# Performance work log

Hardware: AMD Instinct MI355X
Metric: run time of the kernel (lower is better)

Reference implementation:

```python
import jax, jax.numpy as jnp
import numpy as np

N_QUBITS = 10
DIM = 2 ** N_QUBITS
W_MUL = (2.0 ** 0.5) * 5.0 ** (-0.5)  # he_std * lrmul, use_wscale=True, lrmul=1
MEASURE_QUBIT = 5


def _c(v):
    return v.astype(jnp.complex64)


def _m2(a, b, c, d):
    return jnp.stack([jnp.stack([a, b]), jnp.stack([c, d])])


_ZERO = jnp.zeros((), jnp.complex64)


def _rx(phi):
    c, s = _c(jnp.cos(phi / 2)), _c(jnp.sin(phi / 2))
    return _m2(c, -1j * s, -1j * s, c)


def _ry(phi):
    c, s = _c(jnp.cos(phi / 2)), _c(jnp.sin(phi / 2))
    return _m2(c, -s, s, c)


def _rz(phi):
    c, s = _c(jnp.cos(phi / 2)), _c(jnp.sin(phi / 2))
    return _m2(c - 1j * s, _ZERO, _ZERO, c + 1j * s)


_CNOT = jnp.array([[1, 0, 0, 0], [0, 1, 0, 0], [0, 0, 0, 1], [0, 0, 1, 0]], jnp.complex64)


def _expand(g, n, q):
    # kron(I_{2^q}, g, I_{2^{n-q-k}}) where g acts on qubits q..q+k-1
    k = int(np.log2(g.shape[0]))
    left = jnp.eye(2 ** q, dtype=jnp.complex64)
    right = jnp.eye(2 ** (n - q - k), dtype=jnp.complex64)
    return jnp.kron(left, jnp.kron(g, right))


def _layer_unitary(weight):
    w = weight * W_MUL
    U = jnp.eye(DIM, dtype=jnp.complex64)
    for sign in (1.0, -1.0):
        for q in range(N_QUBITS):
            U = _expand(_rx(sign * w[q]), N_QUBITS, q) @ U
            U = _expand(_ry(sign * w[q + 10]), N_QUBITS, q) @ U
            U = _expand(_rz(sign * w[q + 20]), N_QUBITS, q) @ U
        for q in range(1, N_QUBITS):
            U = _expand(_CNOT, N_QUBITS, q - 1) @ U
    return U


def _measure_affinity(rho, which_q):
    # Tr(rho @ Z_which_q) with Z_q = kron(I, Z, I); Z_q is diagonal
    z = jnp.array([1.0, -1.0], jnp.float32)
    zdiag = jnp.kron(jnp.ones(2 ** which_q, jnp.float32),
                     jnp.kron(z, jnp.ones(2 ** (N_QUBITS - which_q - 1), jnp.float32)))
    return jnp.sum(jnp.diagonal(rho).real * zdiag).astype(jnp.float32)


def setup_inputs() -> dict:
    key = jax.random.key(0)
    k1, k2 = jax.random.split(key)
    x = jax.random.normal(k1, (DIM, DIM), dtype=jnp.float32)
    weight = jax.random.uniform(k2, (30,), dtype=jnp.float32, minval=0.0, maxval=2.0 * np.pi)
    return {"x": x, "weight": weight}


def reference(x, weight):
    E = _layer_unitary(weight)
    rho = (E @ x.astype(jnp.complex64)) @ E.conj().T
    return _measure_affinity(rho, MEASURE_QUBIT)
```

## Files before the change

kernel.cpp:

```cpp
#include <hip/hip_runtime.h>

#define DIM 1024
#define NQ 10

__device__ __forceinline__ float2 cmul(float2 a, float2 b) {
    return make_float2(a.x * b.x - a.y * b.y, a.x * b.y + a.y * b.x);
}
__device__ __forceinline__ float2 cadd(float2 a, float2 b) {
    return make_float2(a.x + b.x, a.y + b.y);
}
__device__ __forceinline__ float2 csub(float2 a, float2 b) {
    return make_float2(a.x - b.x, a.y - b.y);
}
__device__ __forceinline__ float2 cconj(float2 a) { return make_float2(a.x, -a.y); }

__device__ __forceinline__ void mm2(const float2* A, const float2* B, float2* C) {
    C[0] = cadd(cmul(A[0], B[0]), cmul(A[1], B[2]));
    C[1] = cadd(cmul(A[0], B[1]), cmul(A[1], B[3]));
    C[2] = cadd(cmul(A[2], B[0]), cmul(A[3], B[2]));
    C[3] = cadd(cmul(A[2], B[1]), cmul(A[3], B[3]));
}

__device__ __forceinline__ void compute_gates(const float* __restrict__ weight,
                                              float2* G, float2* Msh, int tid) {
    if (tid < NQ) {
        int q = tid;
        const float WM = 0.632455532033676f;
        float px = weight[q]      * WM * 0.5f;
        float py = weight[q + 10] * WM * 0.5f;
        float pz = weight[q + 20] * WM * 0.5f;
        float cx = cosf(px), sx = sinf(px);
        float cy = cosf(py), sy = sinf(py);
        float cz = cosf(pz), sz = sinf(pz);
        {
            float2 Rx[4] = { {cx, 0.f}, {0.f, -sx}, {0.f, -sx}, {cx, 0.f} };
            float2 Ry[4] = { {cy, 0.f}, {-sy, 0.f}, {sy, 0.f}, {cy, 0.f} };
            float2 Rz[4] = { {cz, -sz}, {0.f, 0.f}, {0.f, 0.f}, {cz, sz} };
            float2 T[4], u[4];
            mm2(Ry, Rx, T);
            mm2(Rz, T, u);
            G[q * 4 + 0] = u[0]; G[q * 4 + 1] = u[1];
            G[q * 4 + 2] = u[2]; G[q * 4 + 3] = u[3];
        }
        if (Msh && q < 6) {
            float nsx = -sx, nsy = -sy, nsz = -sz;
            float2 Rx[4] = { {cx, 0.f}, {0.f, -nsx}, {0.f, -nsx}, {cx, 0.f} };
            float2 Ry[4] = { {cy, 0.f}, {-nsy, 0.f}, {nsy, 0.f}, {cy, 0.f} };
            float2 Rz[4] = { {cz, -nsz}, {0.f, 0.f}, {0.f, 0.f}, {cz, nsz} };
            float2 T[4], u2[4];
            mm2(Ry, Rx, T);
            mm2(Rz, T, u2);
            for (int i = 0; i < 2; i++)
                for (int j = 0; j < 2; j++) {
                    float2 v = csub(cmul(cconj(u2[0 * 2 + i]), u2[0 * 2 + j]),
                                    cmul(cconj(u2[1 * 2 + i]), u2[1 * 2 + j]));
                    Msh[q * 4 + i * 2 + j] = v;
                }
        }
    }
}

__global__ __launch_bounds__(256) void pass1(const float* __restrict__ x,
                                             const float* __restrict__ weight,
                                             float2* __restrict__ z,
                                             float* __restrict__ out) {
    __shared__ float2 G[40];
    int tid = threadIdx.x;
    compute_gates(weight, G, nullptr, tid);
    __syncthreads();
    if (blockIdx.x == 0 && tid == 0) out[0] = 0.f;

    int lane = tid & 63;
    int r = blockIdx.x * 4 + (tid >> 6);
    const float4* xp = (const float4*)(x + r * DIM + lane * 16);
    float2 v[16];
#pragma unroll
    for (int k = 0; k < 4; k++) {
        float4 a = xp[k];
        v[k * 4 + 0] = make_float2(a.x, 0.f);
        v[k * 4 + 1] = make_float2(a.y, 0.f);
        v[k * 4 + 2] = make_float2(a.z, 0.f);
        v[k * 4 + 3] = make_float2(a.w, 0.f);
    }
#pragma unroll
    for (int q = 0; q < 6; q++) {
        float2 u0 = cconj(G[q * 4]),     u1 = cconj(G[q * 4 + 1]);
        float2 u2 = cconj(G[q * 4 + 2]), u3 = cconj(G[q * 4 + 3]);
        const int X = 1 << (5 - q);
        bool up = (lane & X) != 0;
        float2 go = up ? u3 : u0;
        float2 gp = up ? u2 : u1;
#pragma unroll
        for (int j = 0; j < 16; j++) {
            float2 p;
            p.x = __shfl_xor(v[j].x, X, 64);
            p.y = __shfl_xor(v[j].y, X, 64);
            v[j] = cadd(cmul(go, v[j]), cmul(gp, p));
        }
    }
#pragma unroll
    for (int q = 6; q < 10; q++) {
        float2 u0 = cconj(G[q * 4]),     u1 = cconj(G[q * 4 + 1]);
        float2 u2 = cconj(G[q * 4 + 2]), u3 = cconj(G[q * 4 + 3]);
        const int h = 1 << (9 - q);
#pragma unroll
        for (int j0 = 0; j0 < 16; j0++) {
            if ((j0 & h) == 0) {
                int j1 = j0 | h;
                float2 s0 = v[j0], s1 = v[j1];
                v[j0] = cadd(cmul(u0, s0), cmul(u1, s1));
                v[j1] = cadd(cmul(u2, s0), cmul(u3, s1));
            }
        }
    }
    float4* zp = (float4*)(z + r * DIM + lane * 16);
#pragma unroll
    for (int k = 0; k < 8; k++)
        zp[k] = make_float4(v[2 * k].x, v[2 * k].y, v[2 * k + 1].x, v[2 * k + 1].y);
}

__device__ __forceinline__ float extract_half(int c, const float2 v[8], int half,
                                              int lane, const float2* Msh) {
    int af = c;
    af ^= af >> 1; af ^= af >> 2; af ^= af >> 4; af ^= af >> 8;
    int t = af & 15;
    int a05 = af >> 4;
    float2 m6 = make_float2(1.f, 0.f);
#pragma unroll
    for (int q = 0; q < 6; q++) {
        int ia = (a05 >> (5 - q)) & 1;
        int ib = (lane >> (5 - q)) & 1;
        m6 = cmul(m6, Msh[q * 4 + ia * 2 + ib]);
    }
    int pl = lane;
    pl ^= pl >> 1; pl ^= pl >> 2; pl ^= pl >> 4;
    float acc = 0.f;
#pragma unroll
    for (int jj = 0; jj < 8; jj++) {
        int j = half * 8 + jj;
        int p4j = j ^ (j >> 1) ^ (j >> 2) ^ (j >> 3);
        int parmask = (p4j & 1) ? 63 : 0;
        int bf = (p4j << 6) | (pl ^ parmask);
        int b05 = bf >> 4;
        float mx = __shfl(m6.x, b05, 64);
        float my = __shfl(m6.y, b05, 64);
        if ((bf & 15) == t) acc += mx * v[jj].x - my * v[jj].y;
    }
    return acc;
}

__global__ __launch_bounds__(256) void pass2(const float2* __restrict__ z,
                                             const float* __restrict__ weight,
                                             float* __restrict__ out) {
    __shared__ float2 G[40];
    __shared__ float2 Msh[24];
    __shared__ float2 ex[2 * 2 * 8 * 2 * 64];
    __shared__ float part[4];
    int tid = threadIdx.x;
    int lane = tid & 63;
    int w = tid >> 6;
    int pair = w >> 1;
    int half = w & 1;
    int c0 = blockIdx.x * 4 + pair * 2;

    float2 v0[8], v1[8];
#pragma unroll
    for (int jj = 0; jj < 8; jj++) {
        int j = half * 8 + jj;
        float4 t = *(const float4*)(z + ((j << 6) + lane) * DIM + c0);
        v0[jj] = make_float2(t.x, t.y);
        v1[jj] = make_float2(t.z, t.w);
    }
    compute_gates(weight, G, Msh, tid);
    int sec = pair * 2 + half;
#pragma unroll
    for (int jj = 0; jj < 8; jj++) {
        ex[((sec * 8 + jj) * 2 + 0) * 64 + lane] = v0[jj];
        ex[((sec * 8 + jj) * 2 + 1) * 64 + lane] = v1[jj];
    }
    __syncthreads();
    {
        float2 u0 = G[0], u1 = G[1], u2 = G[2], u3 = G[3];
        float2 go = half ? u3 : u0;
        float2 gp = half ? u2 : u1;
        int other = pair * 2 + (1 - half);
#pragma unroll
        for (int jj = 0; jj < 8; jj++) {
            float2 p0 = ex[((other * 8 + jj) * 2 + 0) * 64 + lane];
            float2 p1 = ex[((other * 8 + jj) * 2 + 1) * 64 + lane];
            v0[jj] = cadd(cmul(go, v0[jj]), cmul(gp, p0));
            v1[jj] = cadd(cmul(go, v1[jj]), cmul(gp, p1));
        }
    }
#pragma unroll
    for (int q = 1; q < 4; q++) {
        float2 u0 = G[q * 4], u1 = G[q * 4 + 1], u2 = G[q * 4 + 2], u3 = G[q * 4 + 3];
        const int h = 8 >> q;
#pragma unroll
        for (int j0 = 0; j0 < 8; j0++) {
            if ((j0 & h) == 0) {
                int j1 = j0 | h;
                {
                    float2 s0 = v0[j0], s1 = v0[j1];
                    v0[j0] = cadd(cmul(u0, s0), cmul(u1, s1));
                    v0[j1] = cadd(cmul(u2, s0), cmul(u3, s1));
                }
                {
                    float2 s0 = v1[j0], s1 = v1[j1];
                    v1[j0] = cadd(cmul(u0, s0), cmul(u1, s1));
                    v1[j1] = cadd(cmul(u2, s0), cmul(u3, s1));
                }
            }
        }
    }
#pragma unroll
    for (int q = 4; q < 10; q++) {
        float2 u0 = G[q * 4], u1 = G[q * 4 + 1], u2 = G[q * 4 + 2], u3 = G[q * 4 + 3];
        const int X = 1 << (9 - q);
        bool up = (lane & X) != 0;
        float2 go = up ? u3 : u0;
        float2 gp = up ? u2 : u1;
#pragma unroll
        for (int jj = 0; jj < 8; jj++) {
            float2 p0, p1;
            p0.x = __shfl_xor(v0[jj].x, X, 64);
            p0.y = __shfl_xor(v0[jj].y, X, 64);
            p1.x = __shfl_xor(v1[jj].x, X, 64);
            p1.y = __shfl_xor(v1[jj].y, X, 64);
            v0[jj] = cadd(cmul(go, v0[jj]), cmul(gp, p0));
            v1[jj] = cadd(cmul(go, v1[jj]), cmul(gp, p1));
        }
    }

    float acc = extract_half(c0, v0, half, lane, Msh) +
                extract_half(c0 + 1, v1, half, lane, Msh);
#pragma unroll
    for (int off = 32; off > 0; off >>= 1) acc += __shfl_xor(acc, off, 64);
    if (lane == 0) part[w] = acc;
    __syncthreads();
    if (tid == 0) atomicAdd(out, part[0] + part[1] + part[2] + part[3]);
}

extern "C" void kernel_launch(void* const* d_in, const int* in_sizes, int n_in,
                              void* d_out, int out_size, void* d_ws, size_t ws_size,
                              hipStream_t stream) {
    const float* x = (const float*)d_in[0];
    const float* weight = (const float*)d_in[1];
    float* out = (float*)d_out;

    float2* z = (float2*)d_ws + 8192;

    pass1<<<256, 256, 0, stream>>>(x, weight, z, out);
    pass2<<<256, 256, 0, stream>>>(z, weight, out);
}
```

Measured before the change: 81.76 us.

## Transpose intermediate in pass1 via shared memory so pass2 reads contiguous rows

Pass1 now uses 512 threads, two waves per row. It applies the first gate through a padded shared-memory transpose and writes the intermediate column-major, so pass2 can read each column as contiguous float4 rows instead of strided gathers. Pass2 likewise splits each column across two waves and replaces the per-element shuffle-based extraction with a closed-form parity selection of a single element per lane. This targets uncoalesced global reads and extraction overhead, at the cost of about 40KB of shared memory per block in pass1 and more complex index logic.

```diff
diff --git a/kernel.cpp b/kernel.cpp
--- a/kernel.cpp
+++ b/kernel.cpp
@@ -60,38 +60,53 @@
     }
 }
 
-__global__ __launch_bounds__(256) void pass1(const float* __restrict__ x,
+__global__ __launch_bounds__(512) void pass1(const float* __restrict__ x,
                                              const float* __restrict__ weight,
-                                             float2* __restrict__ z,
+                                             float2* __restrict__ zt,
                                              float* __restrict__ out) {
     __shared__ float2 G[40];
+    __shared__ float2 sh[DIM * 5];
     int tid = threadIdx.x;
+    int lane = tid & 63;
+    int w = tid >> 6;
+    int rl = w >> 1;
+    int h = w & 1;
+    int r = blockIdx.x * 4 + rl;
+
+    const float* xp = x + r * DIM + (h << 9) + lane;
+    float2 v[8];
+#pragma unroll
+    for (int j = 0; j < 8; j++) v[j] = make_float2(xp[j * 64], 0.f);
+
     compute_gates(weight, G, nullptr, tid);
-    __syncthreads();
     if (blockIdx.x == 0 && tid == 0) out[0] = 0.f;
-
-    int lane = tid & 63;
-    int r = blockIdx.x * 4 + (tid >> 6);
-    const float4* xp = (const float4*)(x + r * DIM + lane * 16);
-    float2 v[16];
-#pragma unroll
-    for (int k = 0; k < 4; k++) {
-        float4 a = xp[k];
-        v[k * 4 + 0] = make_float2(a.x, 0.f);
-        v[k * 4 + 1] = make_float2(a.y, 0.f);
-        v[k * 4 + 2] = make_float2(a.z, 0.f);
-        v[k * 4 + 3] = make_float2(a.w, 0.f);
-    }
-#pragma unroll
-    for (int q = 0; q < 6; q++) {
+    __syncthreads();
+
+#pragma unroll
+    for (int q = 1; q < 4; q++) {
         float2 u0 = cconj(G[q * 4]),     u1 = cconj(G[q * 4 + 1]);
         float2 u2 = cconj(G[q * 4 + 2]), u3 = cconj(G[q * 4 + 3]);
-        const int X = 1 << (5 - q);
+        const int hb = 1 << (3 - q);
+#pragma unroll
+        for (int j0 = 0; j0 < 8; j0++) {
+            if ((j0 & hb) == 0) {
+                int j1 = j0 | hb;
+                float2 s0 = v[j0], s1 = v[j1];
+                v[j0] = cadd(cmul(u0, s0), cmul(u1, s1));
+                v[j1] = cadd(cmul(u2, s0), cmul(u3, s1));
+            }
+        }
+    }
+#pragma unroll
+    for (int q = 4; q < 10; q++) {
+        float2 u0 = cconj(G[q * 4]),     u1 = cconj(G[q * 4 + 1]);
+        float2 u2 = cconj(G[q * 4 + 2]), u3 = cconj(G[q * 4 + 3]);
+        const int X = 1 << (9 - q);
         bool up = (lane & X) != 0;
         float2 go = up ? u3 : u0;
         float2 gp = up ? u2 : u1;
 #pragma unroll
-        for (int j = 0; j < 16; j++) {
+        for (int j = 0; j < 8; j++) {
             float2 p;
             p.x = __shfl_xor(v[j].x, X, 64);
             p.y = __shfl_xor(v[j].y, X, 64);
@@ -99,146 +114,133 @@
         }
     }
 #pragma unroll
-    for (int q = 6; q < 10; q++) {
-        float2 u0 = cconj(G[q * 4]),     u1 = cconj(G[q * 4 + 1]);
-        float2 u2 = cconj(G[q * 4 + 2]), u3 = cconj(G[q * 4 + 3]);
-        const int h = 1 << (9 - q);
-#pragma unroll
-        for (int j0 = 0; j0 < 16; j0++) {
-            if ((j0 & h) == 0) {
-                int j1 = j0 | h;
+    for (int j = 0; j < 8; j++) {
+        int c = (h << 9) | (j << 6) | lane;
+        sh[c * 5 + rl] = v[j];
+    }
+    __syncthreads();
+    {
+        float2 g00 = cconj(G[0]), g01 = cconj(G[1]), g10 = cconj(G[2]), g11 = cconj(G[3]);
+        int cL = tid, cH = tid + 512;
+        int r0 = blockIdx.x * 4;
+        float2 oL[4], oH[4];
+#pragma unroll
+        for (int k = 0; k < 4; k++) {
+            float2 L = sh[cL * 5 + k];
+            float2 H = sh[cH * 5 + k];
+            oL[k] = cadd(cmul(g00, L), cmul(g01, H));
+            oH[k] = cadd(cmul(g10, L), cmul(g11, H));
+        }
+        float4* pL = (float4*)(zt + cL * DIM + r0);
+        float4* pH = (float4*)(zt + cH * DIM + r0);
+        pL[0] = make_float4(oL[0].x, oL[0].y, oL[1].x, oL[1].y);
+        pL[1] = make_float4(oL[2].x, oL[2].y, oL[3].x, oL[3].y);
+        pH[0] = make_float4(oH[0].x, oH[0].y, oH[1].x, oH[1].y);
+        pH[1] = make_float4(oH[2].x, oH[2].y, oH[3].x, oH[3].y);
+    }
+}
+
+__global__ __launch_bounds__(512) void pass2(const float2* __restrict__ zt,
+                                             const float* __restrict__ weight,
+                                             float* __restrict__ out) {
+    __shared__ float2 G[40];
+    __shared__ float2 Msh[24];
+    __shared__ float part[8];
+    int tid = threadIdx.x;
+    int lane = tid & 63;
+    int w = tid >> 6;
+    int pr = w >> 1;
+    int h = w & 1;
+    int c = blockIdx.x * 4 + pr;
+
+    const float4* zp = (const float4*)(zt + c * DIM);
+    const float4* po = zp + h * 256 + lane * 4;
+    const float4* pp = zp + (1 - h) * 256 + lane * 4;
+    float2 a[8], b[8];
+#pragma unroll
+    for (int k = 0; k < 4; k++) {
+        float4 t0 = po[k];
+        a[2 * k]     = make_float2(t0.x, t0.y);
+        a[2 * k + 1] = make_float2(t0.z, t0.w);
+        float4 t1 = pp[k];
+        b[2 * k]     = make_float2(t1.x, t1.y);
+        b[2 * k + 1] = make_float2(t1.z, t1.w);
+    }
+    compute_gates(weight, G, Msh, tid);
+    __syncthreads();
+
+    float2 v[8];
+    {
+        float2 ga = h ? G[3] : G[0];
+        float2 gb = h ? G[2] : G[1];
+#pragma unroll
+        for (int j = 0; j < 8; j++) v[j] = cadd(cmul(ga, a[j]), cmul(gb, b[j]));
+    }
+#pragma unroll
+    for (int q = 1; q < 7; q++) {
+        float2 u0 = G[q * 4], u1 = G[q * 4 + 1], u2 = G[q * 4 + 2], u3 = G[q * 4 + 3];
+        const int X = 1 << (6 - q);
+        bool up = (lane & X) != 0;
+        float2 go = up ? u3 : u0;
+        float2 gp = up ? u2 : u1;
+#pragma unroll
+        for (int j = 0; j < 8; j++) {
+            float2 p;
+            p.x = __shfl_xor(v[j].x, X, 64);
+            p.y = __shfl_xor(v[j].y, X, 64);
+            v[j] = cadd(cmul(go, v[j]), cmul(gp, p));
+        }
+    }
+#pragma unroll
+    for (int q = 7; q < 10; q++) {
+        float2 u0 = G[q * 4], u1 = G[q * 4 + 1], u2 = G[q * 4 + 2], u3 = G[q * 4 + 3];
+        const int hb = 1 << (9 - q);
+#pragma unroll
+        for (int j0 = 0; j0 < 8; j0++) {
+            if ((j0 & hb) == 0) {
+                int j1 = j0 | hb;
                 float2 s0 = v[j0], s1 = v[j1];
                 v[j0] = cadd(cmul(u0, s0), cmul(u1, s1));
                 v[j1] = cadd(cmul(u2, s0), cmul(u3, s1));
             }
         }
     }
-    float4* zp = (float4*)(z + r * DIM + lane * 16);
-#pragma unroll
-    for (int k = 0; k < 8; k++)
-        zp[k] = make_float4(v[2 * k].x, v[2 * k].y, v[2 * k + 1].x, v[2 * k + 1].y);
-}
-
-__device__ __forceinline__ float extract_half(int c, const float2 v[8], int half,
-                                              int lane, const float2* Msh) {
+
     int af = c;
     af ^= af >> 1; af ^= af >> 2; af ^= af >> 4; af ^= af >> 8;
     int t = af & 15;
     int a05 = af >> 4;
+    int p5 = (lane >> 5) & 1;
+    int p4 = p5 ^ ((lane >> 4) & 1);
+    int p3 = p4 ^ ((lane >> 3) & 1);
+    int p2 = p3 ^ ((lane >> 2) & 1);
+    int p1 = p2 ^ ((lane >> 1) & 1);
+    int p0 = p1 ^ (lane & 1);
+    int t3 = (t >> 3) & 1, t2 = (t >> 2) & 1, t1b = (t >> 1) & 1, t0 = t & 1;
+    bool sel = ((h ^ p0) == t3);
+    int jsel = ((t2 ^ t3) << 2) | ((t1b ^ t2) << 1) | (t0 ^ t1b);
+    float2 vs = v[0];
+#pragma unroll
+    for (int j = 1; j < 8; j++) if (jsel == j) vs = v[j];
     float2 m6 = make_float2(1.f, 0.f);
-#pragma unroll
-    for (int q = 0; q < 6; q++) {
-        int ia = (a05 >> (5 - q)) & 1;
-        int ib = (lane >> (5 - q)) & 1;
-        m6 = cmul(m6, Msh[q * 4 + ia * 2 + ib]);
-    }
-    int pl = lane;
-    pl ^= pl >> 1; pl ^= pl >> 2; pl ^= pl >> 4;
-    float acc = 0.f;
-#pragma unroll
-    for (int jj = 0; jj < 8; jj++) {
-        int j = half * 8 + jj;
-        int p4j = j ^ (j >> 1) ^ (j >> 2) ^ (j >> 3);
-        int parmask = (p4j & 1) ? 63 : 0;
-        int bf = (p4j << 6) | (pl ^ parmask);
-        int b05 = bf >> 4;
-        float mx = __shfl(m6.x, b05, 64);
-        float my = __shfl(m6.y, b05, 64);
-        if ((bf & 15) == t) acc += mx * v[jj].x - my * v[jj].y;
-    }
-    return acc;
-}
-
-__global__ __launch_bounds__(256) void pass2(const float2* __restrict__ z,
-                                             const float* __restrict__ weight,
-                                             float* __restrict__ out) {
-    __shared__ float2 G[40];
-    __shared__ float2 Msh[24];
-    __shared__ float2 ex[2 * 2 * 8 * 2 * 64];
-    __shared__ float part[4];
-    int tid = threadIdx.x;
-    int lane = tid & 63;
-    int w = tid >> 6;
-    int pair = w >> 1;
-    int half = w & 1;
-    int c0 = blockIdx.x * 4 + pair * 2;
-
-    float2 v0[8], v1[8];
-#pragma unroll
-    for (int jj = 0; jj < 8; jj++) {
-        int j = half * 8 + jj;
-        float4 t = *(const float4*)(z + ((j << 6) + lane) * DIM + c0);
-        v0[jj] = make_float2(t.x, t.y);
-        v1[jj] = make_float2(t.z, t.w);
-    }
-    compute_gates(weight, G, Msh, tid);
-    int sec = pair * 2 + half;
-#pragma unroll
-    for (int jj = 0; jj < 8; jj++) {
-        ex[((sec * 8 + jj) * 2 + 0) * 64 + lane] = v0[jj];
-        ex[((sec * 8 + jj) * 2 + 1) * 64 + lane] = v1[jj];
-    }
-    __syncthreads();
-    {
-        float2 u0 = G[0], u1 = G[1], u2 = G[2], u3 = G[3];
-        float2 go = half ? u3 : u0;
-        float2 gp = half ? u2 : u1;
-        int other = pair * 2 + (1 - half);
-#pragma unroll
-        for (int jj = 0; jj < 8; jj++) {
-            float2 p0 = ex[((other * 8 + jj) * 2 + 0) * 64 + lane];
-            float2 p1 = ex[((other * 8 + jj) * 2 + 1) * 64 + lane];
-            v0[jj] = cadd(cmul(go, v0[jj]), cmul(gp, p0));
-            v1[jj] = cadd(cmul(go, v1[jj]), cmul(gp, p1));
-        }
-    }
-#pragma unroll
-    for (int q = 1; q < 4; q++) {
-        float2 u0 = G[q * 4], u1 = G[q * 4 + 1], u2 = G[q * 4 + 2], u3 = G[q * 4 + 3];
-        const int h = 8 >> q;
-#pragma unroll
-        for (int j0 = 0; j0 < 8; j0++) {
-            if ((j0 & h) == 0) {
-                int j1 = j0 | h;
-                {
-                    float2 s0 = v0[j0], s1 = v0[j1];
-                    v0[j0] = cadd(cmul(u0, s0), cmul(u1, s1));
-                    v0[j1] = cadd(cmul(u2, s0), cmul(u3, s1));
-                }
-                {
-                    float2 s0 = v1[j0], s1 = v1[j1];
-                    v1[j0] = cadd(cmul(u0, s0), cmul(u1, s1));
-                    v1[j1] = cadd(cmul(u2, s0), cmul(u3, s1));
-                }
-            }
-        }
-    }
-#pragma unroll
-    for (int q = 4; q < 10; q++) {
-        float2 u0 = G[q * 4], u1 = G[q * 4 + 1], u2 = G[q * 4 + 2], u3 = G[q * 4 + 3];
-        const int X = 1 << (9 - q);
-        bool up = (lane & X) != 0;
-        float2 go = up ? u3 : u0;
-        float2 gp = up ? u2 : u1;
-#pragma unroll
-        for (int jj = 0; jj < 8; jj++) {
-            float2 p0, p1;
-            p0.x = __shfl_xor(v0[jj].x, X, 64);
-            p0.y = __shfl_xor(v0[jj].y, X, 64);
-            p1.x = __shfl_xor(v1[jj].x, X, 64);
-            p1.y = __shfl_xor(v1[jj].y, X, 64);
-            v0[jj] = cadd(cmul(go, v0[jj]), cmul(gp, p0));
-            v1[jj] = cadd(cmul(go, v1[jj]), cmul(gp, p1));
-        }
-    }
-
-    float acc = extract_half(c0, v0, half, lane, Msh) +
-                extract_half(c0 + 1, v1, half, lane, Msh);
+    int ib0 = h, ib1 = h ^ p5, ib2 = h ^ p4, ib3 = h ^ p3, ib4 = h ^ p2, ib5 = h ^ p1;
+    m6 = cmul(m6, Msh[0 * 4 + ((a05 >> 5) & 1) * 2 + ib0]);
+    m6 = cmul(m6, Msh[1 * 4 + ((a05 >> 4) & 1) * 2 + ib1]);
+    m6 = cmul(m6, Msh[2 * 4 + ((a05 >> 3) & 1) * 2 + ib2]);
+    m6 = cmul(m6, Msh[3 * 4 + ((a05 >> 2) & 1) * 2 + ib3]);
+    m6 = cmul(m6, Msh[4 * 4 + ((a05 >> 1) & 1) * 2 + ib4]);
+    m6 = cmul(m6, Msh[5 * 4 + (a05 & 1) * 2 + ib5]);
+
+    float acc = sel ? (m6.x * vs.x - m6.y * vs.y) : 0.f;
 #pragma unroll
     for (int off = 32; off > 0; off >>= 1) acc += __shfl_xor(acc, off, 64);
     if (lane == 0) part[w] = acc;
     __syncthreads();
-    if (tid == 0) atomicAdd(out, part[0] + part[1] + part[2] + part[3]);
+    if (tid == 0) {
+        float s = part[0] + part[1] + part[2] + part[3] +
+                  part[4] + part[5] + part[6] + part[7];
+        atomicAdd(out, s);
+    }
 }
 
 extern "C" void kernel_launch(void* const* d_in, const int* in_sizes, int n_in,
@@ -248,8 +250,8 @@
     const float* weight = (const float*)d_in[1];
     float* out = (float*)d_out;
 
-    float2* z = (float2*)d_ws + 8192;
-
-    pass1<<<256, 256, 0, stream>>>(x, weight, z, out);
-    pass2<<<256, 256, 0, stream>>>(z, weight, out);
-}
+    float2* zt = (float2*)d_ws + 8192;
+
+    pass1<<<256, 512, 0, stream>>>(x, weight, zt, out);
+    pass2<<<256, 512, 0, stream>>>(zt, weight, out);
+}
```

Result: faster. 75.36 us (-7.8%).
